# Optimization experiments

Hardware: AMD Instinct MI355X
Metric: run time of the kernel (lower is better)

The kernel has to match this reference:

```python
import jax, jax.numpy as jnp
import numpy as np

EMBED_DIM = 1024
NUM_HEADS = 16
HEAD_DIM = EMBED_DIM // NUM_HEADS


def setup_inputs() -> dict:
    key = jax.random.key(0)
    k1, k2, k3 = jax.random.split(key, 3)
    B, L = 4, 2048
    x = jax.random.normal(k1, (B, L, EMBED_DIM), dtype=jnp.float32)
    # Scale weights like typical init (fan_in variance) to keep logits sane.
    W_qkv = jax.random.normal(k2, (EMBED_DIM, 3 * EMBED_DIM), dtype=jnp.float32) / np.sqrt(EMBED_DIM)
    b_qkv = jnp.zeros((3 * EMBED_DIM,), dtype=jnp.float32)
    W_lin = jax.random.normal(k3, (EMBED_DIM, EMBED_DIM), dtype=jnp.float32) / np.sqrt(EMBED_DIM)
    b_lin = jnp.zeros((EMBED_DIM,), dtype=jnp.float32)
    return {"x": x, "W_qkv": W_qkv, "b_qkv": b_qkv, "W_lin": W_lin, "b_lin": b_lin}


def reference(x, W_qkv, b_qkv, W_lin, b_lin):
    B, L, D = x.shape
    H, Hd = NUM_HEADS, HEAD_DIM
    qkv = x @ W_qkv + b_qkv                      # [B, L, 3D]
    q, k, v = jnp.split(qkv, 3, axis=-1)
    # split heads -> [B, H, L, Hd]
    def split_heads(t):
        return t.reshape(B, L, H, Hd).transpose(0, 2, 1, 3)
    q, k, v = map(split_heads, (q, k, v))
    scores = jnp.einsum("bhqd,bhkd->bhqk", q, k) / jnp.sqrt(jnp.float32(Hd))
    causal = jnp.tril(jnp.ones((L, L), dtype=bool))
    scores = jnp.where(causal, scores, -jnp.inf)
    attn = jax.nn.softmax(scores, axis=-1)
    ctx = jnp.einsum("bhqk,bhkd->bhqd", attn, v)  # [B, H, L, Hd]
    z = ctx.transpose(0, 2, 1, 3).reshape(B, L, D)
    return z @ W_lin + b_lin                      # dropout rate 0 (eval) -> identity
```

## Files before the change

### kernel.cpp

```cpp
#include <hip/hip_runtime.h>
#include <math.h>
#include <stdint.h>


typedef __attribute__((ext_vector_type(8))) short bf16x8;
typedef __attribute__((ext_vector_type(4))) float f32x4;
typedef unsigned short u16;

#define MFMA16(a, b, c) __builtin_amdgcn_mfma_f32_16x16x32_bf16(a, b, c, 0, 0, 0)

__device__ __forceinline__ void bsplit(float x, short& hi, short& lo) {
    unsigned u = __builtin_bit_cast(unsigned, x);
    unsigned hu = u & 0xffff0000u;
    hi = (short)(hu >> 16);
    float r = x - __builtin_bit_cast(float, hu);
    lo = (short)(__builtin_bit_cast(unsigned, r) >> 16);
}

__device__ __forceinline__ void gload16(const void* g, void* l) {
    __builtin_amdgcn_global_load_lds(
        (const __attribute__((address_space(1))) void*)g,
        (__attribute__((address_space(3))) void*)l, 16, 0, 0);
}

__device__ __forceinline__ int swz(int row, int col) {
    return ((row << 6) | col) ^ ((row & 7) << 3);
}

__global__ __launch_bounds__(256) void wsplit_t(
    const float* __restrict__ W, u16* __restrict__ outh, u16* __restrict__ outl,
    int K, int N)
{
    __shared__ float t[64][68];
    const int n0 = blockIdx.x * 64, k0 = blockIdx.y * 64;
    const int tid = threadIdx.x;
    const int r = tid >> 4, c4 = (tid & 15) * 4;
    #pragma unroll
    for (int i = 0; i < 4; ++i) {
        const int rr = r + i * 16;
        float4 v = *(const float4*)&W[(size_t)(k0 + rr) * N + n0 + c4];
        t[rr][c4 + 0] = v.x; t[rr][c4 + 1] = v.y;
        t[rr][c4 + 2] = v.z; t[rr][c4 + 3] = v.w;
    }
    __syncthreads();
    #pragma unroll
    for (int i = 0; i < 4; ++i) {
        const int nr = r + i * 16;
        unsigned h01 = 0, h23 = 0, l01 = 0, l23 = 0;
        {
            short hh, ll;
            bsplit(t[c4 + 0][nr], hh, ll); h01 |= (unsigned)(u16)hh; l01 |= (unsigned)(u16)ll;
            bsplit(t[c4 + 1][nr], hh, ll); h01 |= (unsigned)(u16)hh << 16; l01 |= (unsigned)(u16)ll << 16;
            bsplit(t[c4 + 2][nr], hh, ll); h23 |= (unsigned)(u16)hh; l23 |= (unsigned)(u16)ll;
            bsplit(t[c4 + 3][nr], hh, ll); h23 |= (unsigned)(u16)hh << 16; l23 |= (unsigned)(u16)ll << 16;
        }
        *(uint2*)&outh[(size_t)(n0 + nr) * K + k0 + c4] = make_uint2(h01, h23);
        *(uint2*)&outl[(size_t)(n0 + nr) * K + k0 + c4] = make_uint2(l01, l23);
    }
}

template<bool AF32, bool QKVOUT>
__global__ __launch_bounds__(256) void gemm_split(
    const float* __restrict__ Af,
    const u16* __restrict__ Ah, const u16* __restrict__ Al,
    const u16* __restrict__ Bth, const u16* __restrict__ Btl,
    const float* __restrict__ bias, float* __restrict__ C,
    u16* __restrict__ qh, u16* __restrict__ ql,
    u16* __restrict__ kh, u16* __restrict__ kl,
    u16* __restrict__ vth, u16* __restrict__ vtl,
    int M, int N, int K)
{
    __shared__ u16 sAh[128 * 32], sAl[128 * 32], sBh[128 * 32], sBl[128 * 32];

    const int tid  = threadIdx.x;
    const int lane = tid & 63;
    const int ln   = lane & 15;
    const int lg   = lane >> 4;
    const int w    = tid >> 6;
    const int wr   = (w >> 1) * 64;
    const int wc   = (w & 1) * 64;
    const int row0 = blockIdx.y * 128;
    const int col0 = blockIdx.x * 128;

    f32x4 acc[4][4];
    #pragma unroll
    for (int mi = 0; mi < 4; ++mi)
        #pragma unroll
        for (int ni = 0; ni < 4; ++ni)
            acc[mi][ni] = (f32x4){0.f, 0.f, 0.f, 0.f};

    for (int kt = 0; kt < K; kt += 32) {
        __syncthreads();
        #pragma unroll
        for (int rd = 0; rd < 2; ++rd) {
            const int ch = tid + rd * 256;
            const int r = ch >> 2, kc = (ch & 3) * 8;
            gload16(Bth + (size_t)(col0 + r) * K + kt + kc, &sBh[ch * 8]);
            gload16(Btl + (size_t)(col0 + r) * K + kt + kc, &sBl[ch * 8]);
            if constexpr (!AF32) {
                gload16(Ah + (size_t)(row0 + r) * K + kt + kc, &sAh[ch * 8]);
                gload16(Al + (size_t)(row0 + r) * K + kt + kc, &sAl[ch * 8]);
            }
        }
        if constexpr (AF32) {
            const int r = tid >> 1, ks = (tid & 1) * 16;
            const float* ap = Af + (size_t)(row0 + r) * K + kt + ks;
            float v[16];
            *(float4*)&v[0]  = *(const float4*)(ap + 0);
            *(float4*)&v[4]  = *(const float4*)(ap + 4);
            *(float4*)&v[8]  = *(const float4*)(ap + 8);
            *(float4*)&v[12] = *(const float4*)(ap + 12);
            bf16x8 h0, h1, l0, l1;
            #pragma unroll
            for (int e = 0; e < 8; ++e) {
                short hh, ll;
                bsplit(v[e], hh, ll);     h0[e] = hh; l0[e] = ll;
                bsplit(v[8 + e], hh, ll); h1[e] = hh; l1[e] = ll;
            }
            *(bf16x8*)&sAh[r * 32 + ks]     = h0;
            *(bf16x8*)&sAh[r * 32 + ks + 8] = h1;
            *(bf16x8*)&sAl[r * 32 + ks]     = l0;
            *(bf16x8*)&sAl[r * 32 + ks + 8] = l1;
        }
        __syncthreads();

        bf16x8 a_h[4], a_l[4], b_h[4], b_l[4];
        #pragma unroll
        for (int mi = 0; mi < 4; ++mi) {
            const int o = (wr + mi * 16 + ln) * 32 + lg * 8;
            a_h[mi] = *(const bf16x8*)&sAh[o];
            a_l[mi] = *(const bf16x8*)&sAl[o];
        }
        #pragma unroll
        for (int ni = 0; ni < 4; ++ni) {
            const int o = (wc + ni * 16 + ln) * 32 + lg * 8;
            b_h[ni] = *(const bf16x8*)&sBh[o];
            b_l[ni] = *(const bf16x8*)&sBl[o];
        }
        #pragma unroll
        for (int mi = 0; mi < 4; ++mi)
            #pragma unroll
            for (int ni = 0; ni < 4; ++ni) {
                acc[mi][ni] = MFMA16(a_h[mi], b_h[ni], acc[mi][ni]);
                acc[mi][ni] = MFMA16(a_l[mi], b_h[ni], acc[mi][ni]);
                acc[mi][ni] = MFMA16(a_h[mi], b_l[ni], acc[mi][ni]);
            }
    }

    if constexpr (QKVOUT) {
        const int t = col0 >> 10;
        #pragma unroll
        for (int ni = 0; ni < 4; ++ni) {
            const int col = col0 + wc + ni * 16 + ln;
            const int hh  = (col & 1023) >> 6;
            const int d   = col & 63;
            const float bi = bias[col];
            const size_t hb = (size_t)((row0 >> 11) * 16 + hh);
            #pragma unroll
            for (int mi = 0; mi < 4; ++mi) {
                const int l0g = (row0 + wr + mi * 16 + lg * 4) & 2047;
                if (t == 0) {
                    #pragma unroll
                    for (int j = 0; j < 4; ++j) {
                        short hi_, lo_;
                        bsplit((acc[mi][ni][j] + bi) * 0.125f, hi_, lo_);
                        const size_t p = (hb * 2048 + l0g + j) * 64 + d;
                        qh[p] = (u16)hi_; ql[p] = (u16)lo_;
                    }
                } else if (t == 1) {
                    #pragma unroll
                    for (int j = 0; j < 4; ++j) {
                        short hi_, lo_;
                        bsplit(acc[mi][ni][j] + bi, hi_, lo_);
                        const int l = l0g + j;
                        const size_t p = (hb * 32 + (l >> 6)) * 4096 + swz(l & 63, d);
                        kh[p] = (u16)hi_; kl[p] = (u16)lo_;
                    }
                } else {
                    unsigned h01 = 0, h23 = 0, l01 = 0, l23 = 0;
                    #pragma unroll
                    for (int j = 0; j < 4; ++j) {
                        short hi_, lo_;
                        bsplit(acc[mi][ni][j] + bi, hi_, lo_);
                        if (j < 2) {
                            h01 |= (unsigned)(u16)hi_ << (16 * j);
                            l01 |= (unsigned)(u16)lo_ << (16 * j);
                        } else {
                            h23 |= (unsigned)(u16)hi_ << (16 * (j - 2));
                            l23 |= (unsigned)(u16)lo_ << (16 * (j - 2));
                        }
                    }
                    const size_t p = (hb * 32 + (l0g >> 6)) * 4096 + swz(d, l0g & 63);
                    *(uint2*)&vth[p] = make_uint2(h01, h23);
                    *(uint2*)&vtl[p] = make_uint2(l01, l23);
                }
            }
        }
    } else {
        #pragma unroll
        for (int ni = 0; ni < 4; ++ni) {
            const int col = col0 + wc + ni * 16 + ln;
            const float bi = bias[col];
            #pragma unroll
            for (int mi = 0; mi < 4; ++mi)
                #pragma unroll
                for (int j = 0; j < 4; ++j) {
                    const int row = row0 + wr + mi * 16 + lg * 4 + j;
                    C[(size_t)row * N + col] = acc[mi][ni][j] + bi;
                }
        }
    }
}

__global__ __launch_bounds__(256) void attn_mfma(
    const u16* __restrict__ Qh, const u16* __restrict__ Ql,
    const u16* __restrict__ Kh, const u16* __restrict__ Kl,
    const u16* __restrict__ Vth, const u16* __restrict__ Vtl,
    u16* __restrict__ ctxh, u16* __restrict__ ctxl)
{
    const int L = 2048, D = 1024;
    const int qt = blockIdx.x;
    const int h  = blockIdx.y;
    const int b  = blockIdx.z;
    const int q0 = qt * 64;

    __shared__ u16 sKh[4096], sKl[4096], sVh[4096], sVl[4096];
    __shared__ u16 P_hi[4096], P_lo[4096];

    const int tid = threadIdx.x;
    const int w = tid >> 6;
    const int lane = tid & 63;
    const int ln = lane & 15;
    const int lg = lane >> 4;
    const size_t hb = (size_t)(b * 16 + h);

    bf16x8 qa_hi[2], qa_lo[2];
    {
        const size_t qoff = (hb * 2048 + q0 + w * 16 + ln) * 64 + lg * 8;
        qa_hi[0] = *(const bf16x8*)(Qh + qoff);
        qa_hi[1] = *(const bf16x8*)(Qh + qoff + 32);
        qa_lo[0] = *(const bf16x8*)(Ql + qoff);
        qa_lo[1] = *(const bf16x8*)(Ql + qoff + 32);
    }

    float m[4], lsum[4];
    f32x4 acc[4];
    #pragma unroll
    for (int r = 0; r < 4; ++r) { m[r] = -INFINITY; lsum[r] = 0.f; }
    #pragma unroll
    for (int n = 0; n < 4; ++n) acc[n] = (f32x4){0.f, 0.f, 0.f, 0.f};

    for (int kt = 0; kt <= qt; ++kt) {
        __syncthreads();

        {
            const size_t tb = (hb * 32 + kt) * 4096;
            const int c0 = tid * 8, c1 = (tid + 256) * 8;
            gload16(Kh  + tb + c0, &sKh[c0]);
            gload16(Kh  + tb + c1, &sKh[c1]);
            gload16(Kl  + tb + c0, &sKl[c0]);
            gload16(Kl  + tb + c1, &sKl[c1]);
            gload16(Vth + tb + c0, &sVh[c0]);
            gload16(Vth + tb + c1, &sVh[c1]);
            gload16(Vtl + tb + c0, &sVl[c0]);
            gload16(Vtl + tb + c1, &sVl[c1]);
        }
        __syncthreads();

        f32x4 s[4];
        #pragma unroll
        for (int n = 0; n < 4; ++n) {
            f32x4 sa = (f32x4){0.f, 0.f, 0.f, 0.f};
            #pragma unroll
            for (int ks = 0; ks < 2; ++ks) {
                bf16x8 kb_hi = *(const bf16x8*)&sKh[swz(n * 16 + ln, ks * 32 + lg * 8)];
                bf16x8 kb_lo = *(const bf16x8*)&sKl[swz(n * 16 + ln, ks * 32 + lg * 8)];
                sa = MFMA16(qa_hi[ks], kb_hi, sa);
                sa = MFMA16(qa_lo[ks], kb_hi, sa);
                sa = MFMA16(qa_hi[ks], kb_lo, sa);
            }
            s[n] = sa;
        }

        if (kt == qt) {
            #pragma unroll
            for (int n = 0; n < 4; ++n)
                #pragma unroll
                for (int r = 0; r < 4; ++r) {
                    const int key = n * 16 + ln;
                    const int qr  = w * 16 + lg * 4 + r;
                    if (key > qr) s[n][r] = -INFINITY;
                }
        }

        float al[4];
        #pragma unroll
        for (int r = 0; r < 4; ++r) {
            float t = fmaxf(fmaxf(s[0][r], s[1][r]), fmaxf(s[2][r], s[3][r]));
            t = fmaxf(t, __shfl_xor(t, 1));
            t = fmaxf(t, __shfl_xor(t, 2));
            t = fmaxf(t, __shfl_xor(t, 4));
            t = fmaxf(t, __shfl_xor(t, 8));
            const float mn = fmaxf(m[r], t);
            al[r] = __expf(m[r] - mn);
            m[r] = mn;
        }

        float ps[4] = {0.f, 0.f, 0.f, 0.f};
        #pragma unroll
        for (int n = 0; n < 4; ++n) {
            #pragma unroll
            for (int r = 0; r < 4; ++r) {
                const float p = __expf(s[n][r] - m[r]);
                ps[r] += p;
                short ph, pl;
                bsplit(p, ph, pl);
                const int row = w * 16 + lg * 4 + r;
                const int key = n * 16 + ln;
                P_hi[swz(row, key)] = (u16)ph;
                P_lo[swz(row, key)] = (u16)pl;
            }
        }
        #pragma unroll
        for (int r = 0; r < 4; ++r) {
            float t = ps[r];
            t += __shfl_xor(t, 1);
            t += __shfl_xor(t, 2);
            t += __shfl_xor(t, 4);
            t += __shfl_xor(t, 8);
            lsum[r] = lsum[r] * al[r] + t;
            acc[0][r] *= al[r];
            acc[1][r] *= al[r];
            acc[2][r] *= al[r];
            acc[3][r] *= al[r];
        }

        bf16x8 pa_hi[2], pa_lo[2];
        #pragma unroll
        for (int ks = 0; ks < 2; ++ks) {
            pa_hi[ks] = *(const bf16x8*)&P_hi[swz(w * 16 + ln, ks * 32 + lg * 8)];
            pa_lo[ks] = *(const bf16x8*)&P_lo[swz(w * 16 + ln, ks * 32 + lg * 8)];
        }
        #pragma unroll
        for (int n = 0; n < 4; ++n) {
            #pragma unroll
            for (int ks = 0; ks < 2; ++ks) {
                bf16x8 vb_hi = *(const bf16x8*)&sVh[swz(n * 16 + ln, ks * 32 + lg * 8)];
                bf16x8 vb_lo = *(const bf16x8*)&sVl[swz(n * 16 + ln, ks * 32 + lg * 8)];
                acc[n] = MFMA16(pa_hi[ks], vb_hi, acc[n]);
                acc[n] = MFMA16(pa_lo[ks], vb_hi, acc[n]);
                acc[n] = MFMA16(pa_hi[ks], vb_lo, acc[n]);
            }
        }
    }

    #pragma unroll
    for (int r = 0; r < 4; ++r) {
        const float inv = 1.f / lsum[r];
        const int q = q0 + w * 16 + lg * 4 + r;
        const size_t idx = ((size_t)(b * L) + q) * D + h * 64;
        #pragma unroll
        for (int n = 0; n < 4; ++n) {
            short hh, ll;
            bsplit(acc[n][r] * inv, hh, ll);
            ctxh[idx + n * 16 + ln] = (u16)hh;
            ctxl[idx + n * 16 + ln] = (u16)ll;
        }
    }
}

extern "C" void kernel_launch(void* const* d_in, const int* in_sizes, int n_in,
                              void* d_out, int out_size, void* d_ws, size_t ws_size,
                              hipStream_t stream) {
    const float* x     = (const float*)d_in[0];
    const float* W_qkv = (const float*)d_in[1];
    const float* b_qkv = (const float*)d_in[2];
    const float* W_lin = (const float*)d_in[3];
    const float* b_lin = (const float*)d_in[4];
    float* out = (float*)d_out;

    const int M = 8192, D = 1024, D3 = 3072;
    const size_t MB = 1024 * 1024;

    char* ws = (char*)d_ws;
    u16* Qh  = (u16*)(ws + 0 * MB);
    u16* Ql  = (u16*)(ws + 16 * MB);
    u16* Kh  = (u16*)(ws + 32 * MB);
    u16* Kl  = (u16*)(ws + 48 * MB);
    u16* Vth = (u16*)(ws + 64 * MB);
    u16* Vtl = (u16*)(ws + 80 * MB);
    u16* wqh = (u16*)(ws + 96 * MB);
    u16* wql = (u16*)(ws + 102 * MB);
    u16* ctxh = (u16*)(ws + 96 * MB);
    u16* ctxl = (u16*)(ws + 112 * MB);
    u16* wlh = (u16*)(ws + 0 * MB);
    u16* wll = (u16*)(ws + 2 * MB);

    wsplit_t<<<dim3(D3 / 64, D / 64), 256, 0, stream>>>(W_qkv, wqh, wql, D, D3);
    gemm_split<true, true><<<dim3(D3 / 128, M / 128), 256, 0, stream>>>(
        x, nullptr, nullptr, wqh, wql, b_qkv, nullptr,
        Qh, Ql, Kh, Kl, Vth, Vtl, M, D3, D);
    attn_mfma<<<dim3(32, 16, 4), 256, 0, stream>>>(
        Qh, Ql, Kh, Kl, Vth, Vtl, ctxh, ctxl);
    wsplit_t<<<dim3(D / 64, D / 64), 256, 0, stream>>>(W_lin, wlh, wll, D, D);
    gemm_split<false, false><<<dim3(D / 128, M / 128), 256, 0, stream>>>(
        nullptr, ctxh, ctxl, wlh, wll, b_lin, out,
        nullptr, nullptr, nullptr, nullptr, nullptr, nullptr, M, D, D);
}
```

Baseline: 659.2 us.

## Double-buffer K/V tiles in attention kernel with async LDS prefetch

Splits the K/V shared-memory tiles into two buffers and issues the global-to-LDS loads for the next key tile before computing on the current one. Explicit vmcnt waits and barriers replace the two __syncthreads per iteration, so load latency can overlap with the QK and PV MFMA work. This doubles K/V LDS usage, which may lower occupancy, and relies on the manual waitcnt counts being correct.

```diff
diff --git a/kernel.cpp b/kernel.cpp
--- a/kernel.cpp
+++ b/kernel.cpp
@@ -224,7 +224,7 @@
     const int b  = blockIdx.z;
     const int q0 = qt * 64;
 
-    __shared__ u16 sKh[4096], sKl[4096], sVh[4096], sVl[4096];
+    __shared__ u16 sKh[2][4096], sKl[2][4096], sVh[2][4096], sVl[2][4096];
     __shared__ u16 P_hi[4096], P_lo[4096];
 
     const int tid = threadIdx.x;
@@ -243,6 +243,19 @@
         qa_lo[1] = *(const bf16x8*)(Ql + qoff + 32);
     }
 
+    const int c0 = tid * 8, c1 = (tid + 256) * 8;
+    auto stage = [&](int buf, int kt) {
+        const size_t tb = (hb * 32 + kt) * 4096;
+        gload16(Kh  + tb + c0, &sKh[buf][c0]);
+        gload16(Kh  + tb + c1, &sKh[buf][c1]);
+        gload16(Kl  + tb + c0, &sKl[buf][c0]);
+        gload16(Kl  + tb + c1, &sKl[buf][c1]);
+        gload16(Vth + tb + c0, &sVh[buf][c0]);
+        gload16(Vth + tb + c1, &sVh[buf][c1]);
+        gload16(Vtl + tb + c0, &sVl[buf][c0]);
+        gload16(Vtl + tb + c1, &sVl[buf][c1]);
+    };
+
     float m[4], lsum[4];
     f32x4 acc[4];
     #pragma unroll
@@ -250,22 +263,19 @@
     #pragma unroll
     for (int n = 0; n < 4; ++n) acc[n] = (f32x4){0.f, 0.f, 0.f, 0.f};
 
+    stage(0, 0);
+
     for (int kt = 0; kt <= qt; ++kt) {
-        __syncthreads();
-
-        {
-            const size_t tb = (hb * 32 + kt) * 4096;
-            const int c0 = tid * 8, c1 = (tid + 256) * 8;
-            gload16(Kh  + tb + c0, &sKh[c0]);
-            gload16(Kh  + tb + c1, &sKh[c1]);
-            gload16(Kl  + tb + c0, &sKl[c0]);
-            gload16(Kl  + tb + c1, &sKl[c1]);
-            gload16(Vth + tb + c0, &sVh[c0]);
-            gload16(Vth + tb + c1, &sVh[c1]);
-            gload16(Vtl + tb + c0, &sVl[c0]);
-            gload16(Vtl + tb + c1, &sVl[c1]);
-        }
-        __syncthreads();
+        const int cur = kt & 1;
+        if (kt < qt) {
+            stage(cur ^ 1, kt + 1);
+            asm volatile("s_waitcnt vmcnt(8)" ::: "memory");
+        } else {
+            asm volatile("s_waitcnt vmcnt(0)" ::: "memory");
+        }
+        __builtin_amdgcn_sched_barrier(0);
+        __builtin_amdgcn_s_barrier();
+        asm volatile("" ::: "memory");
 
         f32x4 s[4];
         #pragma unroll
@@ -273,8 +283,8 @@
             f32x4 sa = (f32x4){0.f, 0.f, 0.f, 0.f};
             #pragma unroll
             for (int ks = 0; ks < 2; ++ks) {
-                bf16x8 kb_hi = *(const bf16x8*)&sKh[swz(n * 16 + ln, ks * 32 + lg * 8)];
-                bf16x8 kb_lo = *(const bf16x8*)&sKl[swz(n * 16 + ln, ks * 32 + lg * 8)];
+                bf16x8 kb_hi = *(const bf16x8*)&sKh[cur][swz(n * 16 + ln, ks * 32 + lg * 8)];
+                bf16x8 kb_lo = *(const bf16x8*)&sKl[cur][swz(n * 16 + ln, ks * 32 + lg * 8)];
                 sa = MFMA16(qa_hi[ks], kb_hi, sa);
                 sa = MFMA16(qa_lo[ks], kb_hi, sa);
                 sa = MFMA16(qa_hi[ks], kb_lo, sa);
@@ -345,13 +355,16 @@
         for (int n = 0; n < 4; ++n) {
             #pragma unroll
             for (int ks = 0; ks < 2; ++ks) {
-                bf16x8 vb_hi = *(const bf16x8*)&sVh[swz(n * 16 + ln, ks * 32 + lg * 8)];
-                bf16x8 vb_lo = *(const bf16x8*)&sVl[swz(n * 16 + ln, ks * 32 + lg * 8)];
+                bf16x8 vb_hi = *(const bf16x8*)&sVh[cur][swz(n * 16 + ln, ks * 32 + lg * 8)];
+                bf16x8 vb_lo = *(const bf16x8*)&sVl[cur][swz(n * 16 + ln, ks * 32 + lg * 8)];
                 acc[n] = MFMA16(pa_hi[ks], vb_hi, acc[n]);
                 acc[n] = MFMA16(pa_lo[ks], vb_hi, acc[n]);
                 acc[n] = MFMA16(pa_hi[ks], vb_lo, acc[n]);
             }
         }
+
+        asm volatile("" ::: "memory");
+        __builtin_amdgcn_s_barrier();
     }
 
     #pragma unroll
```

Result: no change. 664.9 us (+0.9%).

## Compute transposed attention scores to keep P in registers, dropping LDS round-trip

Applied to the files above, without the earlier changes.

The attention kernel now computes S^T by swapping MFMA operand order, so each lane holds one query row's scores across keys. P can then be split into hi/lo bf16 and fed straight into the PV MFMA as the B operand, with no write to shared memory. The V^T layout written by the QKV GEMM is permuted (vslot) so that key order matches the register layout of P. This also removes the P shared buffers, shortens the row reductions to two shuffles, and packs context stores into 8-byte writes. The cost is a changed data layout that the producer and consumer kernels must agree on exactly.

```diff
diff --git a/kernel.cpp b/kernel.cpp
--- a/kernel.cpp
+++ b/kernel.cpp
@@ -25,6 +25,10 @@
 
 __device__ __forceinline__ int swz(int row, int col) {
     return ((row << 6) | col) ^ ((row & 7) << 3);
+}
+
+__device__ __forceinline__ int vslot(int kk) {
+    return (kk & 32) | ((kk & 12) << 1) | ((kk & 16) >> 2) | (kk & 3);
 }
 
 __global__ __launch_bounds__(256) void wsplit_t(
@@ -190,7 +194,8 @@
                             l23 |= (unsigned)(u16)lo_ << (16 * (j - 2));
                         }
                     }
-                    const size_t p = (hb * 32 + (l0g >> 6)) * 4096 + swz(d, l0g & 63);
+                    const int s0 = vslot(l0g & 63);
+                    const size_t p = (hb * 32 + (l0g >> 6)) * 4096 + swz(d, s0);
                     *(uint2*)&vth[p] = make_uint2(h01, h23);
                     *(uint2*)&vtl[p] = make_uint2(l01, l23);
                 }
@@ -225,7 +230,6 @@
     const int q0 = qt * 64;
 
     __shared__ u16 sKh[4096], sKl[4096], sVh[4096], sVl[4096];
-    __shared__ u16 P_hi[4096], P_lo[4096];
 
     const int tid = threadIdx.x;
     const int w = tid >> 6;
@@ -234,28 +238,26 @@
     const int lg = lane >> 4;
     const size_t hb = (size_t)(b * 16 + h);
 
-    bf16x8 qa_hi[2], qa_lo[2];
+    bf16x8 qb_hi[2], qb_lo[2];
     {
         const size_t qoff = (hb * 2048 + q0 + w * 16 + ln) * 64 + lg * 8;
-        qa_hi[0] = *(const bf16x8*)(Qh + qoff);
-        qa_hi[1] = *(const bf16x8*)(Qh + qoff + 32);
-        qa_lo[0] = *(const bf16x8*)(Ql + qoff);
-        qa_lo[1] = *(const bf16x8*)(Ql + qoff + 32);
-    }
-
-    float m[4], lsum[4];
+        qb_hi[0] = *(const bf16x8*)(Qh + qoff);
+        qb_hi[1] = *(const bf16x8*)(Qh + qoff + 32);
+        qb_lo[0] = *(const bf16x8*)(Ql + qoff);
+        qb_lo[1] = *(const bf16x8*)(Ql + qoff + 32);
+    }
+
+    float m = -INFINITY, lsum = 0.f;
     f32x4 acc[4];
     #pragma unroll
-    for (int r = 0; r < 4; ++r) { m[r] = -INFINITY; lsum[r] = 0.f; }
-    #pragma unroll
     for (int n = 0; n < 4; ++n) acc[n] = (f32x4){0.f, 0.f, 0.f, 0.f};
+
+    const int c0 = tid * 8, c1 = (tid + 256) * 8;
 
     for (int kt = 0; kt <= qt; ++kt) {
         __syncthreads();
-
         {
             const size_t tb = (hb * 32 + kt) * 4096;
-            const int c0 = tid * 8, c1 = (tid + 256) * 8;
             gload16(Kh  + tb + c0, &sKh[c0]);
             gload16(Kh  + tb + c1, &sKh[c1]);
             gload16(Kl  + tb + c0, &sKl[c0]);
@@ -275,97 +277,94 @@
             for (int ks = 0; ks < 2; ++ks) {
                 bf16x8 kb_hi = *(const bf16x8*)&sKh[swz(n * 16 + ln, ks * 32 + lg * 8)];
                 bf16x8 kb_lo = *(const bf16x8*)&sKl[swz(n * 16 + ln, ks * 32 + lg * 8)];
-                sa = MFMA16(qa_hi[ks], kb_hi, sa);
-                sa = MFMA16(qa_lo[ks], kb_hi, sa);
-                sa = MFMA16(qa_hi[ks], kb_lo, sa);
+                sa = MFMA16(kb_hi, qb_hi[ks], sa);
+                sa = MFMA16(kb_lo, qb_hi[ks], sa);
+                sa = MFMA16(kb_hi, qb_lo[ks], sa);
             }
             s[n] = sa;
         }
 
         if (kt == qt) {
+            const int qloc = w * 16 + ln;
             #pragma unroll
             for (int n = 0; n < 4; ++n)
                 #pragma unroll
-                for (int r = 0; r < 4; ++r) {
-                    const int key = n * 16 + ln;
-                    const int qr  = w * 16 + lg * 4 + r;
-                    if (key > qr) s[n][r] = -INFINITY;
-                }
-        }
-
-        float al[4];
-        #pragma unroll
-        for (int r = 0; r < 4; ++r) {
-            float t = fmaxf(fmaxf(s[0][r], s[1][r]), fmaxf(s[2][r], s[3][r]));
-            t = fmaxf(t, __shfl_xor(t, 1));
-            t = fmaxf(t, __shfl_xor(t, 2));
-            t = fmaxf(t, __shfl_xor(t, 4));
-            t = fmaxf(t, __shfl_xor(t, 8));
-            const float mn = fmaxf(m[r], t);
-            al[r] = __expf(m[r] - mn);
-            m[r] = mn;
-        }
-
-        float ps[4] = {0.f, 0.f, 0.f, 0.f};
+                for (int r = 0; r < 4; ++r)
+                    if (n * 16 + lg * 4 + r > qloc) s[n][r] = -INFINITY;
+        }
+
+        float t0 = fmaxf(fmaxf(s[0][0], s[0][1]), fmaxf(s[0][2], s[0][3]));
+        float t1 = fmaxf(fmaxf(s[1][0], s[1][1]), fmaxf(s[1][2], s[1][3]));
+        float t2 = fmaxf(fmaxf(s[2][0], s[2][1]), fmaxf(s[2][2], s[2][3]));
+        float t3 = fmaxf(fmaxf(s[3][0], s[3][1]), fmaxf(s[3][2], s[3][3]));
+        float t = fmaxf(fmaxf(t0, t1), fmaxf(t2, t3));
+        t = fmaxf(t, __shfl_xor(t, 16));
+        t = fmaxf(t, __shfl_xor(t, 32));
+        const float mn = fmaxf(m, t);
+        const float al = __expf(m - mn);
+        m = mn;
+
+        float ps = 0.f;
+        #pragma unroll
+        for (int n = 0; n < 4; ++n)
+            #pragma unroll
+            for (int r = 0; r < 4; ++r) {
+                s[n][r] = __expf(s[n][r] - mn);
+                ps += s[n][r];
+            }
+        ps += __shfl_xor(ps, 16);
+        ps += __shfl_xor(ps, 32);
+        lsum = lsum * al + ps;
         #pragma unroll
         for (int n = 0; n < 4; ++n) {
-            #pragma unroll
-            for (int r = 0; r < 4; ++r) {
-                const float p = __expf(s[n][r] - m[r]);
-                ps[r] += p;
-                short ph, pl;
-                bsplit(p, ph, pl);
-                const int row = w * 16 + lg * 4 + r;
-                const int key = n * 16 + ln;
-                P_hi[swz(row, key)] = (u16)ph;
-                P_lo[swz(row, key)] = (u16)pl;
-            }
-        }
-        #pragma unroll
-        for (int r = 0; r < 4; ++r) {
-            float t = ps[r];
-            t += __shfl_xor(t, 1);
-            t += __shfl_xor(t, 2);
-            t += __shfl_xor(t, 4);
-            t += __shfl_xor(t, 8);
-            lsum[r] = lsum[r] * al[r] + t;
-            acc[0][r] *= al[r];
-            acc[1][r] *= al[r];
-            acc[2][r] *= al[r];
-            acc[3][r] *= al[r];
-        }
-
-        bf16x8 pa_hi[2], pa_lo[2];
-        #pragma unroll
-        for (int ks = 0; ks < 2; ++ks) {
-            pa_hi[ks] = *(const bf16x8*)&P_hi[swz(w * 16 + ln, ks * 32 + lg * 8)];
-            pa_lo[ks] = *(const bf16x8*)&P_lo[swz(w * 16 + ln, ks * 32 + lg * 8)];
-        }
+            acc[n][0] *= al; acc[n][1] *= al;
+            acc[n][2] *= al; acc[n][3] *= al;
+        }
+
+        bf16x8 pb_hi[2], pb_lo[2];
+        #pragma unroll
+        for (int ks = 0; ks < 2; ++ks)
+            #pragma unroll
+            for (int e = 0; e < 8; ++e) {
+                short hh, ll;
+                bsplit(s[2 * ks + (e >> 2)][e & 3], hh, ll);
+                pb_hi[ks][e] = hh;
+                pb_lo[ks][e] = ll;
+            }
+
         #pragma unroll
         for (int n = 0; n < 4; ++n) {
             #pragma unroll
             for (int ks = 0; ks < 2; ++ks) {
                 bf16x8 vb_hi = *(const bf16x8*)&sVh[swz(n * 16 + ln, ks * 32 + lg * 8)];
                 bf16x8 vb_lo = *(const bf16x8*)&sVl[swz(n * 16 + ln, ks * 32 + lg * 8)];
-                acc[n] = MFMA16(pa_hi[ks], vb_hi, acc[n]);
-                acc[n] = MFMA16(pa_lo[ks], vb_hi, acc[n]);
-                acc[n] = MFMA16(pa_hi[ks], vb_lo, acc[n]);
-            }
-        }
-    }
-
+                acc[n] = MFMA16(vb_hi, pb_hi[ks], acc[n]);
+                acc[n] = MFMA16(vb_lo, pb_hi[ks], acc[n]);
+                acc[n] = MFMA16(vb_hi, pb_lo[ks], acc[n]);
+            }
+        }
+    }
+
+    const float inv = 1.f / lsum;
+    const int q = q0 + w * 16 + ln;
+    const size_t base = ((size_t)(b * L) + q) * D + h * 64;
     #pragma unroll
-    for (int r = 0; r < 4; ++r) {
-        const float inv = 1.f / lsum[r];
-        const int q = q0 + w * 16 + lg * 4 + r;
-        const size_t idx = ((size_t)(b * L) + q) * D + h * 64;
-        #pragma unroll
-        for (int n = 0; n < 4; ++n) {
+    for (int n = 0; n < 4; ++n) {
+        unsigned h01 = 0, h23 = 0, l01 = 0, l23 = 0;
+        #pragma unroll
+        for (int r = 0; r < 4; ++r) {
             short hh, ll;
             bsplit(acc[n][r] * inv, hh, ll);
-            ctxh[idx + n * 16 + ln] = (u16)hh;
-            ctxl[idx + n * 16 + ln] = (u16)ll;
-        }
+            if (r < 2) {
+                h01 |= (unsigned)(u16)hh << (16 * r);
+                l01 |= (unsigned)(u16)ll << (16 * r);
+            } else {
+                h23 |= (unsigned)(u16)hh << (16 * (r - 2));
+                l23 |= (unsigned)(u16)ll << (16 * (r - 2));
+            }
+        }
+        *(uint2*)&ctxh[base + n * 16 + lg * 4] = make_uint2(h01, h23);
+        *(uint2*)&ctxl[base + n * 16 + lg * 4] = make_uint2(l01, l23);
     }
 }
 
```

After: 529.7 us. 1.24x faster.
